# Performance work log

Hardware: AMD Instinct MI355X
Metric: run time of the kernel (lower is better)

The kernel has to match this reference:

```python
import jax, jax.numpy as jnp
import numpy as np

G, NI, EI = 10000, 32, 128        # inner graphs, nodes/graph, edges/graph
EO = 160000                        # outer edges
F_IN, H, F_G, NC = 64, 128, 128, 32


def gcn_conv(h, src, dst, n_nodes, W, b):
    # DGL GraphConv, norm='both': D^-1/2 A D^-1/2 h W + b (degree from dst)
    deg = jax.ops.segment_sum(jnp.ones(src.shape[0], h.dtype), dst, num_segments=n_nodes)
    norm = jnp.where(deg > 0, deg, 1.0) ** -0.5
    msg = h[src] * norm[src, None]                       # [E, F]
    agg = jax.ops.segment_sum(msg, dst, num_segments=n_nodes) * norm[:, None]
    return agg @ W + b


def gcn_stack(h, src, dst, n_nodes, params):
    n = len(params)
    for i, (W, b) in enumerate(params):
        h = gcn_conv(h, src, dst, n_nodes, W, b)
        if i < n - 1:
            h = jax.nn.relu(h)
    return h


def setup_inputs() -> dict:
    key = jax.random.key(0)
    ks = jax.random.split(key, 20)
    inp = {
        'inner_features': jax.random.normal(ks[0], (G, NI, F_IN), jnp.float32),
        'inner_src': jax.random.randint(ks[1], (G, EI), 0, NI, jnp.int32),
        'inner_dst': jax.random.randint(ks[2], (G, EI), 0, NI, jnp.int32),
        'outer_src': jax.random.randint(ks[3], (EO,), 0, G, jnp.int32),
        'outer_dst': jax.random.randint(ks[4], (EO,), 0, G, jnp.int32),
    }
    def lin(k, fi, fo):
        s = 1.0 / np.sqrt(fi)
        return jax.random.uniform(k, (fi, fo), jnp.float32, -s, s)
    # inner GCN: F_IN -> H -> H -> F_G
    inp['Wi0'], inp['bi0'] = lin(ks[5], F_IN, H), jnp.zeros((H,), jnp.float32)
    inp['Wi1'], inp['bi1'] = lin(ks[6], H, H), jnp.zeros((H,), jnp.float32)
    inp['Wi2'], inp['bi2'] = lin(ks[7], H, F_G), jnp.zeros((F_G,), jnp.float32)
    # outer GCN: F_G -> H -> H -> NC
    inp['Wo0'], inp['bo0'] = lin(ks[8], F_G, H), jnp.zeros((H,), jnp.float32)
    inp['Wo1'], inp['bo1'] = lin(ks[9], H, H), jnp.zeros((H,), jnp.float32)
    inp['Wo2'], inp['bo2'] = lin(ks[10], H, NC), jnp.zeros((NC,), jnp.float32)
    return inp


def reference(inner_features, inner_src, inner_dst, outer_src, outer_dst,
              Wi0, bi0, Wi1, bi1, Wi2, bi2, Wo0, bo0, Wo1, bo1, Wo2, bo2):
    inner_params = [(Wi0, bi0), (Wi1, bi1), (Wi2, bi2)]
    outer_params = [(Wo0, bo0), (Wo1, bo1), (Wo2, bo2)]
    # vectorized replacement for the per-inner-graph Python loop
    h_inner = jax.vmap(lambda h, s, d: gcn_stack(h, s, d, NI, inner_params))(
        inner_features, inner_src, inner_dst)          # [G, NI, F_G]
    features_new = jnp.mean(h_inner, axis=1)           # torch.mean(h, dim=0) per graph -> [G, F_G]
    return gcn_stack(features_new, outer_src, outer_dst, G, outer_params)  # [G, NC]
```

## Files before the change

kernel.cpp:

```cpp
#include <hip/hip_runtime.h>
#include <math.h>


constexpr int G_N  = 10000;
constexpr int NI_N = 32;
constexpr int EI_N = 128;
constexpr int EO_N = 160000;
constexpr int FIN  = 64;
constexpr int HD   = 128;
constexpr int NCLS = 32;

typedef short bf16x8 __attribute__((ext_vector_type(8)));
typedef float f32x4  __attribute__((ext_vector_type(4)));

#define MFMA16(a, b, c) __builtin_amdgcn_mfma_f32_16x16x32_bf16((a), (b), (c), 0, 0, 0)

__device__ __forceinline__ unsigned short f2bf(float x) {
  unsigned int u = __builtin_bit_cast(unsigned int, x);
  u += 0x7fffu + ((u >> 16) & 1u);
  return (unsigned short)(u >> 16);
}
__device__ __forceinline__ float bflo(unsigned u) {
  return __builtin_bit_cast(float, u << 16);
}
__device__ __forceinline__ float bfhi(unsigned u) {
  return __builtin_bit_cast(float, u & 0xffff0000u);
}

__global__ __launch_bounds__(256) void pack_all_w(
    const float* __restrict__ W0, const float* __restrict__ W1,
    const float* __restrict__ W2, short* __restrict__ o0,
    short* __restrict__ o1, short* __restrict__ o2) {
  const int b = blockIdx.x;
  const float* W; short* out; int K, idx;
  if (b < 4)       { W = W0; out = o0; K = 64;  idx = b * 256 + threadIdx.x; }
  else if (b < 12) { W = W1; out = o1; K = 128; idx = (b - 4) * 256 + threadIdx.x; }
  else             { W = W2; out = o2; K = 128; idx = (b - 12) * 256 + threadIdx.x; }
  const int KB = K >> 5;
  const int lane = idx & 63;
  const int ctkb = idx >> 6;
  const int kb = ctkb % KB;
  const int ct = ctkb / KB;
  const int col = 16 * ct + (lane & 15);
  const int k0 = 32 * kb + 8 * (lane >> 4);
#pragma unroll
  for (int j = 0; j < 8; ++j)
    out[idx * 8 + j] = (short)f2bf(W[(k0 + j) * HD + col]);
}

template <int NCT, bool RELU, bool LAST>
__device__ __forceinline__ void gcn_layer_w(
    int l, const short* __restrict__ sMp, short* __restrict__ sH,
    short* __restrict__ sT, const short* __restrict__ Wp,
    const float* __restrict__ bias, unsigned short* __restrict__ outp) {
  constexpr int KB = NCT / 2;
  const int lg = l >> 4, c15 = l & 15, jj = l & 7;
  const f32x4 z = {0.f, 0.f, 0.f, 0.f};

#pragma unroll
  for (int rt = 0; rt < 2; ++rt) {
    const bf16x8 am = *(const bf16x8*)&sMp[(rt * 64 + l) * 8];
#pragma unroll
    for (int ct = 0; ct < NCT; ++ct) {
      const bf16x8 bh = *(const bf16x8*)&sH[(ct * 64 + l) * 8];
      f32x4 d = MFMA16(am, bh, z);
      const int kb = ct >> 1;
      const int hi = ((ct & 1) << 1) | (c15 >> 3);
      const int base = ((rt * 4 + kb) * 64 + 16 * hi + 4 * lg) * 8 + jj;
#pragma unroll
      for (int r = 0; r < 4; ++r) sT[base + r * 8] = (short)f2bf(d[r]);
    }
  }

  bf16x8 a0[KB], a1[KB];
#pragma unroll
  for (int kb = 0; kb < KB; ++kb) {
    a0[kb] = *(const bf16x8*)&sT[((0 + kb) * 64 + l) * 8];
    a1[kb] = *(const bf16x8*)&sT[((4 + kb) * 64 + l) * 8];
  }
  float pool[8];
#pragma unroll
  for (int ct2 = 0; ct2 < 8; ++ct2) {
    f32x4 acc0 = z, acc1 = z;
#pragma unroll
    for (int kb = 0; kb < KB; ++kb) {
      const bf16x8 bw = *(const bf16x8*)&Wp[((ct2 * KB + kb) * 64 + l) * 8];
      acc0 = MFMA16(a0[kb], bw, acc0);
      acc1 = MFMA16(a1[kb], bw, acc1);
    }
    const float bv = bias[16 * ct2 + c15];
    if (LAST) {
      pool[ct2] = (acc0[0] + acc0[1] + acc0[2] + acc0[3]) +
                  (acc1[0] + acc1[1] + acc1[2] + acc1[3]) + 8.f * bv;
    } else {
      {
        float v0 = acc0[0] + bv, v1 = acc0[1] + bv, v2 = acc0[2] + bv, v3 = acc0[3] + bv;
        if (RELU) { v0 = fmaxf(v0, 0.f); v1 = fmaxf(v1, 0.f);
                    v2 = fmaxf(v2, 0.f); v3 = fmaxf(v3, 0.f); }
        const ushort4 pk = make_ushort4(f2bf(v0), f2bf(v1), f2bf(v2), f2bf(v3));
        const int g2 = (lg >> 1);
        *(ushort4*)&sH[(ct2 * 64 + c15 + 16 * g2) * 8 + 4 * (lg & 1)] = pk;
      }
      {
        float v0 = acc1[0] + bv, v1 = acc1[1] + bv, v2 = acc1[2] + bv, v3 = acc1[3] + bv;
        if (RELU) { v0 = fmaxf(v0, 0.f); v1 = fmaxf(v1, 0.f);
                    v2 = fmaxf(v2, 0.f); v3 = fmaxf(v3, 0.f); }
        const ushort4 pk = make_ushort4(f2bf(v0), f2bf(v1), f2bf(v2), f2bf(v3));
        const int g2 = 2 + (lg >> 1);
        *(ushort4*)&sH[(ct2 * 64 + c15 + 16 * g2) * 8 + 4 * (lg & 1)] = pk;
      }
    }
  }
  if (LAST) {
#pragma unroll
    for (int ct2 = 0; ct2 < 8; ++ct2) {
      float p = pool[ct2];
      p += __shfl_xor(p, 16);
      p += __shfl_xor(p, 32);
      if (l < 16) outp[16 * ct2 + c15] = f2bf(p * (1.0f / NI_N));
    }
  }
}

__global__ __launch_bounds__(64) void inner_gcn_kernel(
    const float* __restrict__ feats, const int* __restrict__ src,
    const int* __restrict__ dst,
    const short* __restrict__ wp0, const float* __restrict__ bi0,
    const short* __restrict__ wp1, const float* __restrict__ bi1,
    const short* __restrict__ wp2, const float* __restrict__ bi2,
    unsigned short* __restrict__ feat_out) {
  __shared__ __align__(16) short sH[8 * 64 * 8];
  __shared__ __align__(16) short sT[8 * 64 * 8];
  __shared__ __align__(16) short sMp[2 * 64 * 8];
  __shared__ float sNorm[NI_N];

  const int l = threadIdx.x;
  const int gid = blockIdx.x;
  const int lg = l >> 4, c15 = l & 15;
  float* sMf = (float*)sT;

  const float4* f4 = (const float4*)(feats + (size_t)gid * (NI_N * FIN));
  float4 hv[8];
#pragma unroll
  for (int it = 0; it < 8; ++it) hv[it] = f4[it * 64 + l];

  const int2 es = ((const int2*)(src + gid * EI_N))[l];
  const int2 ed = ((const int2*)(dst + gid * EI_N))[l];

#pragma unroll
  for (int i = 0; i < 18; ++i) sMf[i * 64 + l] = 0.f;
  atomicAdd(&sMf[ed.x * 36 + es.x], 1.0f);
  atomicAdd(&sMf[ed.y * 36 + es.y], 1.0f);

  {
    const int row = l & 31;
    const float* pr = &sMf[row * 36 + (l >> 5) * 16];
    const float4 q0 = *(const float4*)(pr + 0);
    const float4 q1 = *(const float4*)(pr + 4);
    const float4 q2 = *(const float4*)(pr + 8);
    const float4 q3 = *(const float4*)(pr + 12);
    float p = (q0.x + q0.y + q0.z + q0.w) + (q1.x + q1.y + q1.z + q1.w) +
              (q2.x + q2.y + q2.z + q2.w) + (q3.x + q3.y + q3.z + q3.w);
    p += __shfl_xor(p, 32);
    if (l < 32) sNorm[l] = (p > 0.f) ? (1.0f / sqrtf(p)) : 1.0f;
  }

  {
    const int k0 = 8 * lg;
    const float4 n0 = *(const float4*)&sNorm[k0];
    const float4 n1 = *(const float4*)&sNorm[k0 + 4];
#pragma unroll
    for (int rb = 0; rb < 2; ++rb) {
      const int row = 16 * rb + c15;
      const float nr = sNorm[row];
      const float4 a = *(const float4*)&sMf[row * 36 + k0];
      const float4 b = *(const float4*)&sMf[row * 36 + k0 + 4];
      bf16x8 o;
      o[0] = (short)f2bf(a.x * nr * n0.x); o[1] = (short)f2bf(a.y * nr * n0.y);
      o[2] = (short)f2bf(a.z * nr * n0.z); o[3] = (short)f2bf(a.w * nr * n0.w);
      o[4] = (short)f2bf(b.x * nr * n1.x); o[5] = (short)f2bf(b.y * nr * n1.y);
      o[6] = (short)f2bf(b.z * nr * n1.z); o[7] = (short)f2bf(b.w * nr * n1.w);
      *(bf16x8*)&sMp[(rb * 64 + l) * 8] = o;
    }
  }

#pragma unroll
  for (int it = 0; it < 8; ++it) {
    const int n = it * 4 + lg;
    const int ct = c15 >> 2;
    const int c0 = (c15 & 3) * 4;
    const int lanebase = 16 * (n >> 3);
    const int jj = n & 7;
    const float4 v = hv[it];
    sH[(ct * 64 + c0 + 0 + lanebase) * 8 + jj] = (short)f2bf(v.x);
    sH[(ct * 64 + c0 + 1 + lanebase) * 8 + jj] = (short)f2bf(v.y);
    sH[(ct * 64 + c0 + 2 + lanebase) * 8 + jj] = (short)f2bf(v.z);
    sH[(ct * 64 + c0 + 3 + lanebase) * 8 + jj] = (short)f2bf(v.w);
  }

  gcn_layer_w<4, true, false>(l, sMp, sH, sT, wp0, bi0, nullptr);
  gcn_layer_w<8, true, false>(l, sMp, sH, sT, wp1, bi1, nullptr);
  gcn_layer_w<8, false, true>(l, sMp, sH, sT, wp2, bi2,
                              feat_out + (size_t)gid * HD);
}

__global__ __launch_bounds__(256) void hist_kernel(const int* __restrict__ dst,
                                                   int* __restrict__ degi) {
  const int e = blockIdx.x * 256 + threadIdx.x;
  if (e < EO_N) atomicAdd(&degi[dst[e]], 1);
}

__global__ __launch_bounds__(1024) void scan_norm_kernel(
    const int* __restrict__ degi, int* __restrict__ start,
    int* __restrict__ cursor, float* __restrict__ nrm) {
  __shared__ int part[1024];
  const int t = threadIdx.x;
  const int base = t * 10;
  int loc[10];
  int s = 0;
#pragma unroll
  for (int k = 0; k < 10; ++k) {
    const int i = base + k;
    const int d = (i < G_N) ? degi[i] : 0;
    loc[k] = s;
    s += d;
  }
  part[t] = s;
  __syncthreads();
  for (int off = 1; off < 1024; off <<= 1) {
    const int v = (t >= off) ? part[t - off] : 0;
    __syncthreads();
    part[t] += v;
    __syncthreads();
  }
  const int excl = (t == 0) ? 0 : part[t - 1];
#pragma unroll
  for (int k = 0; k < 10; ++k) {
    const int i = base + k;
    if (i < G_N) {
      const int st = excl + loc[k];
      start[i] = st;
      cursor[i] = st;
      const int d = degi[i];
      nrm[i] = (d > 0) ? (1.0f / sqrtf((float)d)) : 1.0f;
    }
  }
}

__global__ __launch_bounds__(256) void fill_kernel(const int* __restrict__ src,
                                                   const int* __restrict__ dst,
                                                   int* __restrict__ cursor,
                                                   int* __restrict__ esrc) {
  const int e = blockIdx.x * 256 + threadIdx.x;
  if (e < EO_N) {
    const int pos = atomicAdd(&cursor[dst[e]], 1);
    esrc[pos] = src[e];
  }
}

template <int Nout, bool RELU, bool OUTBF>
__global__ __launch_bounds__(256) void gather_mm_kernel(
    const unsigned short* __restrict__ h, const int* __restrict__ esrc,
    const int* __restrict__ start, const int* __restrict__ degi,
    const float* __restrict__ nrm, const float* __restrict__ W,
    const float* __restrict__ bias, void* __restrict__ outv) {
  __shared__ __align__(16) float sIn[16 * HD];
  const int t = threadIdx.x;
  const int row0 = blockIdx.x * 16;
  const int rr = t >> 4, sub = t & 15;
  const int ehalf = sub >> 3, fq = sub & 7;
  const int row = row0 + rr;
  float4 a0 = {0,0,0,0}, a1 = {0,0,0,0}, a2 = {0,0,0,0}, a3 = {0,0,0,0};
  {
    const int s0 = start[row];
    const int cnt = degi[row];
    const unsigned short* hb = h + (size_t)fq * 16;
    for (int i = ehalf; i < cnt; i += 2) {
      const int s = esrc[s0 + i];
      const float ns = nrm[s];
      const unsigned short* p = hb + (size_t)s * HD;
      const uint4 u0 = *(const uint4*)(p);
      const uint4 u1 = *(const uint4*)(p + 8);
      a0.x = fmaf(bflo(u0.x), ns, a0.x); a0.y = fmaf(bfhi(u0.x), ns, a0.y);
      a0.z = fmaf(bflo(u0.y), ns, a0.z); a0.w = fmaf(bfhi(u0.y), ns, a0.w);
      a1.x = fmaf(bflo(u0.z), ns, a1.x); a1.y = fmaf(bfhi(u0.z), ns, a1.y);
      a1.z = fmaf(bflo(u0.w), ns, a1.z); a1.w = fmaf(bfhi(u0.w), ns, a1.w);
      a2.x = fmaf(bflo(u1.x), ns, a2.x); a2.y = fmaf(bfhi(u1.x), ns, a2.y);
      a2.z = fmaf(bflo(u1.y), ns, a2.z); a2.w = fmaf(bfhi(u1.y), ns, a2.w);
      a3.x = fmaf(bflo(u1.z), ns, a3.x); a3.y = fmaf(bfhi(u1.z), ns, a3.y);
      a3.z = fmaf(bflo(u1.w), ns, a3.z); a3.w = fmaf(bfhi(u1.w), ns, a3.w);
    }
  }
  float* q = &sIn[rr * HD + fq * 16];
  if (ehalf == 0) {
    *(float4*)(q + 0) = a0; *(float4*)(q + 4) = a1;
    *(float4*)(q + 8) = a2; *(float4*)(q + 12) = a3;
  }
  __syncthreads();
  if (ehalf == 1) {
    const float nr = nrm[row];
    float4 b0 = *(const float4*)(q + 0), b1 = *(const float4*)(q + 4);
    float4 b2 = *(const float4*)(q + 8), b3 = *(const float4*)(q + 12);
    b0.x = (b0.x + a0.x) * nr; b0.y = (b0.y + a0.y) * nr;
    b0.z = (b0.z + a0.z) * nr; b0.w = (b0.w + a0.w) * nr;
    b1.x = (b1.x + a1.x) * nr; b1.y = (b1.y + a1.y) * nr;
    b1.z = (b1.z + a1.z) * nr; b1.w = (b1.w + a1.w) * nr;
    b2.x = (b2.x + a2.x) * nr; b2.y = (b2.y + a2.y) * nr;
    b2.z = (b2.z + a2.z) * nr; b2.w = (b2.w + a2.w) * nr;
    b3.x = (b3.x + a3.x) * nr; b3.y = (b3.y + a3.y) * nr;
    b3.z = (b3.z + a3.z) * nr; b3.w = (b3.w + a3.w) * nr;
    *(float4*)(q + 0) = b0; *(float4*)(q + 4) = b1;
    *(float4*)(q + 8) = b2; *(float4*)(q + 12) = b3;
  }
  __syncthreads();
  constexpr int NC4 = Nout / 4;
  constexpr int TILES = 4 * NC4;
  if (t < TILES) {
    const int r = t / NC4, c = t % NC4;
    float acc[4][4] = {};
#pragma unroll 8
    for (int k = 0; k < HD; ++k) {
      const float4 wv = *(const float4*)&W[k * Nout + c * 4];
      const float a0s = sIn[(r * 4 + 0) * HD + k];
      const float a1s = sIn[(r * 4 + 1) * HD + k];
      const float a2s = sIn[(r * 4 + 2) * HD + k];
      const float a3s = sIn[(r * 4 + 3) * HD + k];
      acc[0][0] = fmaf(a0s, wv.x, acc[0][0]);
      acc[0][1] = fmaf(a0s, wv.y, acc[0][1]);
      acc[0][2] = fmaf(a0s, wv.z, acc[0][2]);
      acc[0][3] = fmaf(a0s, wv.w, acc[0][3]);
      acc[1][0] = fmaf(a1s, wv.x, acc[1][0]);
      acc[1][1] = fmaf(a1s, wv.y, acc[1][1]);
      acc[1][2] = fmaf(a1s, wv.z, acc[1][2]);
      acc[1][3] = fmaf(a1s, wv.w, acc[1][3]);
      acc[2][0] = fmaf(a2s, wv.x, acc[2][0]);
      acc[2][1] = fmaf(a2s, wv.y, acc[2][1]);
      acc[2][2] = fmaf(a2s, wv.z, acc[2][2]);
      acc[2][3] = fmaf(a2s, wv.w, acc[2][3]);
      acc[3][0] = fmaf(a3s, wv.x, acc[3][0]);
      acc[3][1] = fmaf(a3s, wv.y, acc[3][1]);
      acc[3][2] = fmaf(a3s, wv.z, acc[3][2]);
      acc[3][3] = fmaf(a3s, wv.w, acc[3][3]);
    }
    const float4 bv = *(const float4*)&bias[c * 4];
#pragma unroll
    for (int i = 0; i < 4; ++i) {
      float4 v = make_float4(acc[i][0] + bv.x, acc[i][1] + bv.y,
                             acc[i][2] + bv.z, acc[i][3] + bv.w);
      if (RELU) {
        v.x = fmaxf(v.x, 0.f); v.y = fmaxf(v.y, 0.f);
        v.z = fmaxf(v.z, 0.f); v.w = fmaxf(v.w, 0.f);
      }
      const size_t off = (size_t)(row0 + r * 4 + i) * Nout + c * 4;
      if (OUTBF) {
        const ushort4 o = make_ushort4(f2bf(v.x), f2bf(v.y), f2bf(v.z), f2bf(v.w));
        *(ushort4*)&((unsigned short*)outv)[off] = o;
      } else {
        *(float4*)&((float*)outv)[off] = v;
      }
    }
  }
}

extern "C" void kernel_launch(void* const* d_in, const int* in_sizes, int n_in,
                              void* d_out, int out_size, void* d_ws,
                              size_t ws_size, hipStream_t stream) {
  const float* feats = (const float*)d_in[0];
  const int* isrc = (const int*)d_in[1];
  const int* idst = (const int*)d_in[2];
  const int* osrc = (const int*)d_in[3];
  const int* odst = (const int*)d_in[4];
  const float* Wi0 = (const float*)d_in[5];
  const float* bi0 = (const float*)d_in[6];
  const float* Wi1 = (const float*)d_in[7];
  const float* bi1 = (const float*)d_in[8];
  const float* Wi2 = (const float*)d_in[9];
  const float* bi2 = (const float*)d_in[10];
  const float* Wo0 = (const float*)d_in[11];
  const float* bo0 = (const float*)d_in[12];
  const float* Wo1 = (const float*)d_in[13];
  const float* bo1 = (const float*)d_in[14];
  const float* Wo2 = (const float*)d_in[15];
  const float* bo2 = (const float*)d_in[16];
  float* out = (float*)d_out;

  float* ws = (float*)d_ws;
  unsigned short* feat = (unsigned short*)ws;
  unsigned short* h0 = (unsigned short*)(ws + (size_t)G_N * HD);
  float* nrm  = ws + (size_t)3 * G_N * HD;
  int* degi   = (int*)(ws + (size_t)3 * G_N * HD + G_N);
  int* start  = degi + G_N;
  int* cursor = start + G_N;
  int* esrc   = cursor + G_N;
  short* wp0  = (short*)(esrc + EO_N);
  short* wp1  = wp0 + 8 * 2 * 64 * 8;
  short* wp2  = wp1 + 8 * 4 * 64 * 8;

  pack_all_w<<<20, 256, 0, stream>>>(Wi0, Wi1, Wi2, wp0, wp1, wp2);

  inner_gcn_kernel<<<G_N, 64, 0, stream>>>(feats, isrc, idst, wp0, bi0, wp1,
                                           bi1, wp2, bi2, feat);

  hipMemsetAsync(degi, 0, G_N * sizeof(int), stream);
  hist_kernel<<<(EO_N + 255) / 256, 256, 0, stream>>>(odst, degi);
  scan_norm_kernel<<<1, 1024, 0, stream>>>(degi, start, cursor, nrm);
  fill_kernel<<<(EO_N + 255) / 256, 256, 0, stream>>>(osrc, odst, cursor, esrc);

  const int gm_grid = G_N / 16;
  gather_mm_kernel<HD, true, true><<<gm_grid, 256, 0, stream>>>(
      feat, esrc, start, degi, nrm, Wo0, bo0, h0);
  gather_mm_kernel<HD, true, true><<<gm_grid, 256, 0, stream>>>(
      h0, esrc, start, degi, nrm, Wo1, bo1, feat);
  gather_mm_kernel<NCLS, false, false><<<gm_grid, 256, 0, stream>>>(
      feat, esrc, start, degi, nrm, Wo2, bo2, out);
}
```

Baseline: 175.4 us.

## Fuse outer GCN pipeline into one cooperative persistent kernel with grid syncs

Replaces the memset, histogram, scan, fill and three gather-matmul launches for the outer graph with a single cooperative kernel of 512 persistent blocks. Grid-wide syncs separate the phases, and the per-tile gather code is factored into a device function that each block loops over. The intent is to remove launch gaps and the single-block scan tail between stages. In exchange, grid.sync carries its own cost, the work is spread over fewer blocks, and the old multi-kernel path is kept as a fallback if the cooperative launch fails.

```diff
diff --git a/kernel.cpp b/kernel.cpp
--- a/kernel.cpp
+++ b/kernel.cpp
@@ -1,6 +1,9 @@
 #include <hip/hip_runtime.h>
+#include <hip/hip_cooperative_groups.h>
 #include <math.h>
 
+
+namespace cg = cooperative_groups;
 
 constexpr int G_N  = 10000;
 constexpr int NI_N = 32;
@@ -204,69 +207,14 @@
                               feat_out + (size_t)gid * HD);
 }
 
-__global__ __launch_bounds__(256) void hist_kernel(const int* __restrict__ dst,
-                                                   int* __restrict__ degi) {
-  const int e = blockIdx.x * 256 + threadIdx.x;
-  if (e < EO_N) atomicAdd(&degi[dst[e]], 1);
-}
-
-__global__ __launch_bounds__(1024) void scan_norm_kernel(
-    const int* __restrict__ degi, int* __restrict__ start,
-    int* __restrict__ cursor, float* __restrict__ nrm) {
-  __shared__ int part[1024];
-  const int t = threadIdx.x;
-  const int base = t * 10;
-  int loc[10];
-  int s = 0;
-#pragma unroll
-  for (int k = 0; k < 10; ++k) {
-    const int i = base + k;
-    const int d = (i < G_N) ? degi[i] : 0;
-    loc[k] = s;
-    s += d;
-  }
-  part[t] = s;
-  __syncthreads();
-  for (int off = 1; off < 1024; off <<= 1) {
-    const int v = (t >= off) ? part[t - off] : 0;
-    __syncthreads();
-    part[t] += v;
-    __syncthreads();
-  }
-  const int excl = (t == 0) ? 0 : part[t - 1];
-#pragma unroll
-  for (int k = 0; k < 10; ++k) {
-    const int i = base + k;
-    if (i < G_N) {
-      const int st = excl + loc[k];
-      start[i] = st;
-      cursor[i] = st;
-      const int d = degi[i];
-      nrm[i] = (d > 0) ? (1.0f / sqrtf((float)d)) : 1.0f;
-    }
-  }
-}
-
-__global__ __launch_bounds__(256) void fill_kernel(const int* __restrict__ src,
-                                                   const int* __restrict__ dst,
-                                                   int* __restrict__ cursor,
-                                                   int* __restrict__ esrc) {
-  const int e = blockIdx.x * 256 + threadIdx.x;
-  if (e < EO_N) {
-    const int pos = atomicAdd(&cursor[dst[e]], 1);
-    esrc[pos] = src[e];
-  }
-}
-
 template <int Nout, bool RELU, bool OUTBF>
-__global__ __launch_bounds__(256) void gather_mm_kernel(
-    const unsigned short* __restrict__ h, const int* __restrict__ esrc,
-    const int* __restrict__ start, const int* __restrict__ degi,
-    const float* __restrict__ nrm, const float* __restrict__ W,
-    const float* __restrict__ bias, void* __restrict__ outv) {
-  __shared__ __align__(16) float sIn[16 * HD];
-  const int t = threadIdx.x;
-  const int row0 = blockIdx.x * 16;
+__device__ __forceinline__ void gather_tile(
+    int tile, int t, const unsigned short* __restrict__ h,
+    const int* __restrict__ esrc, const int* __restrict__ start,
+    const int* __restrict__ degi, const float* __restrict__ nrm,
+    const float* __restrict__ W, const float* __restrict__ bias,
+    void* __restrict__ outv, float* __restrict__ sIn) {
+  const int row0 = tile * 16;
   const int rr = t >> 4, sub = t & 15;
   const int ehalf = sub >> 3, fq = sub & 7;
   const int row = row0 + rr;
@@ -362,6 +310,142 @@
   }
 }
 
+__global__ __launch_bounds__(256) void hist_kernel(const int* __restrict__ dst,
+                                                   int* __restrict__ degi) {
+  const int e = blockIdx.x * 256 + threadIdx.x;
+  if (e < EO_N) atomicAdd(&degi[dst[e]], 1);
+}
+
+__global__ __launch_bounds__(1024) void scan_norm_kernel(
+    const int* __restrict__ degi, int* __restrict__ start,
+    int* __restrict__ cursor, float* __restrict__ nrm) {
+  __shared__ int part[1024];
+  const int t = threadIdx.x;
+  const int base = t * 10;
+  int loc[10];
+  int s = 0;
+#pragma unroll
+  for (int k = 0; k < 10; ++k) {
+    const int i = base + k;
+    const int d = (i < G_N) ? degi[i] : 0;
+    loc[k] = s;
+    s += d;
+  }
+  part[t] = s;
+  __syncthreads();
+  for (int off = 1; off < 1024; off <<= 1) {
+    const int v = (t >= off) ? part[t - off] : 0;
+    __syncthreads();
+    part[t] += v;
+    __syncthreads();
+  }
+  const int excl = (t == 0) ? 0 : part[t - 1];
+#pragma unroll
+  for (int k = 0; k < 10; ++k) {
+    const int i = base + k;
+    if (i < G_N) {
+      const int st = excl + loc[k];
+      start[i] = st;
+      cursor[i] = st;
+      const int d = degi[i];
+      nrm[i] = (d > 0) ? (1.0f / sqrtf((float)d)) : 1.0f;
+    }
+  }
+}
+
+__global__ __launch_bounds__(256) void fill_kernel(const int* __restrict__ src,
+                                                   const int* __restrict__ dst,
+                                                   int* __restrict__ cursor,
+                                                   int* __restrict__ esrc) {
+  const int e = blockIdx.x * 256 + threadIdx.x;
+  if (e < EO_N) {
+    const int pos = atomicAdd(&cursor[dst[e]], 1);
+    esrc[pos] = src[e];
+  }
+}
+
+template <int Nout, bool RELU, bool OUTBF>
+__global__ __launch_bounds__(256) void gather_mm_kernel(
+    const unsigned short* __restrict__ h, const int* __restrict__ esrc,
+    const int* __restrict__ start, const int* __restrict__ degi,
+    const float* __restrict__ nrm, const float* __restrict__ W,
+    const float* __restrict__ bias, void* __restrict__ outv) {
+  __shared__ __align__(16) float sIn[16 * HD];
+  gather_tile<Nout, RELU, OUTBF>(blockIdx.x, threadIdx.x, h, esrc, start, degi,
+                                 nrm, W, bias, outv, sIn);
+}
+
+__global__ __launch_bounds__(256, 2) void outer_mega_kernel(
+    unsigned short* feat, unsigned short* h0, float* nrm, int* degi,
+    int* start, int* cursor, int* esrc, const int* osrc, const int* odst,
+    const float* Wo0, const float* bo0, const float* Wo1, const float* bo1,
+    const float* Wo2, const float* bo2, float* out) {
+  cg::grid_group grid = cg::this_grid();
+  __shared__ __align__(16) float sIn[16 * HD];
+  __shared__ int part[256];
+  const int t = threadIdx.x, bid = blockIdx.x;
+  const int nb = gridDim.x;
+  const int gsz = nb * 256;
+
+  for (int i = bid * 256 + t; i < G_N; i += gsz) degi[i] = 0;
+  grid.sync();
+  for (int e = bid * 256 + t; e < EO_N; e += gsz) atomicAdd(&degi[odst[e]], 1);
+  grid.sync();
+  if (bid == 0) {
+    const int base = t * 40;
+    int s = 0;
+    for (int k = 0; k < 40; ++k) {
+      const int i = base + k;
+      s += (i < G_N) ? degi[i] : 0;
+    }
+    part[t] = s;
+    __syncthreads();
+    for (int off = 1; off < 256; off <<= 1) {
+      const int v = (t >= off) ? part[t - off] : 0;
+      __syncthreads();
+      part[t] += v;
+      __syncthreads();
+    }
+    int run = (t == 0) ? 0 : part[t - 1];
+    for (int k = 0; k < 40; ++k) {
+      const int i = base + k;
+      if (i < G_N) {
+        start[i] = run;
+        cursor[i] = run;
+        run += degi[i];
+      }
+    }
+  } else {
+    for (int i = (bid - 1) * 256 + t; i < G_N; i += gsz - 256) {
+      const int d = degi[i];
+      nrm[i] = (d > 0) ? (1.0f / sqrtf((float)d)) : 1.0f;
+    }
+  }
+  grid.sync();
+  for (int e = bid * 256 + t; e < EO_N; e += gsz) {
+    const int pos = atomicAdd(&cursor[odst[e]], 1);
+    esrc[pos] = osrc[e];
+  }
+  grid.sync();
+  for (int tile = bid; tile < G_N / 16; tile += nb) {
+    gather_tile<HD, true, true>(tile, t, feat, esrc, start, degi, nrm, Wo0,
+                                bo0, h0, sIn);
+    __syncthreads();
+  }
+  grid.sync();
+  for (int tile = bid; tile < G_N / 16; tile += nb) {
+    gather_tile<HD, true, true>(tile, t, h0, esrc, start, degi, nrm, Wo1, bo1,
+                                feat, sIn);
+    __syncthreads();
+  }
+  grid.sync();
+  for (int tile = bid; tile < G_N / 16; tile += nb) {
+    gather_tile<NCLS, false, false>(tile, t, feat, esrc, start, degi, nrm, Wo2,
+                                    bo2, out, sIn);
+    __syncthreads();
+  }
+}
+
 extern "C" void kernel_launch(void* const* d_in, const int* in_sizes, int n_in,
                               void* d_out, int out_size, void* d_ws,
                               size_t ws_size, hipStream_t stream) {
@@ -401,16 +485,24 @@
   inner_gcn_kernel<<<G_N, 64, 0, stream>>>(feats, isrc, idst, wp0, bi0, wp1,
                                            bi1, wp2, bi2, feat);
 
-  hipMemsetAsync(degi, 0, G_N * sizeof(int), stream);
-  hist_kernel<<<(EO_N + 255) / 256, 256, 0, stream>>>(odst, degi);
-  scan_norm_kernel<<<1, 1024, 0, stream>>>(degi, start, cursor, nrm);
-  fill_kernel<<<(EO_N + 255) / 256, 256, 0, stream>>>(osrc, odst, cursor, esrc);
-
-  const int gm_grid = G_N / 16;
-  gather_mm_kernel<HD, true, true><<<gm_grid, 256, 0, stream>>>(
-      feat, esrc, start, degi, nrm, Wo0, bo0, h0);
-  gather_mm_kernel<HD, true, true><<<gm_grid, 256, 0, stream>>>(
-      h0, esrc, start, degi, nrm, Wo1, bo1, feat);
-  gather_mm_kernel<NCLS, false, false><<<gm_grid, 256, 0, stream>>>(
-      feat, esrc, start, degi, nrm, Wo2, bo2, out);
-}
+  void* args[] = {&feat, &h0, &nrm, &degi, &start, &cursor, &esrc,
+                  (void*)&osrc, (void*)&odst, (void*)&Wo0, (void*)&bo0,
+                  (void*)&Wo1, (void*)&bo1, (void*)&Wo2, (void*)&bo2, &out};
+  const hipError_t cerr = hipLaunchCooperativeKernel(
+      (const void*)outer_mega_kernel, dim3(512), dim3(256), args, 0, stream);
+
+  if (cerr != hipSuccess) {
+    (void)hipGetLastError();
+    hipMemsetAsync(degi, 0, G_N * sizeof(int), stream);
+    hist_kernel<<<(EO_N + 255) / 256, 256, 0, stream>>>(odst, degi);
+    scan_norm_kernel<<<1, 1024, 0, stream>>>(degi, start, cursor, nrm);
+    fill_kernel<<<(EO_N + 255) / 256, 256, 0, stream>>>(osrc, odst, cursor, esrc);
+    const int gm_grid = G_N / 16;
+    gather_mm_kernel<HD, true, true><<<gm_grid, 256, 0, stream>>>(
+        feat, esrc, start, degi, nrm, Wo0, bo0, h0);
+    gather_mm_kernel<HD, true, true><<<gm_grid, 256, 0, stream>>>(
+        h0, esrc, start, degi, nrm, Wo1, bo1, feat);
+    gather_mm_kernel<NCLS, false, false><<<gm_grid, 256, 0, stream>>>(
+        feat, esrc, start, degi, nrm, Wo2, bo2, out);
+  }
+}
```

Measured after the change: 541.1 us. 209% more time.
